# Kernel tuning notes

Hardware: AMD Instinct MI355X
Metric: run time of the kernel (lower is better)

## Reference

```python
import jax, jax.numpy as jnp
import numpy as np

B, LI, LC, H = 16, 2048, 2048, 1024


def setup_inputs() -> dict:
    key = jax.random.key(0)
    k1, k2, k3, k4 = jax.random.split(key, 4)
    inp = jax.random.normal(k1, (B, LI, H), dtype=jnp.float32)
    ctx = jax.random.normal(k2, (B, LC, H), dtype=jnp.float32)
    # mask out the last quarter of context positions (True = masked), never a full row
    context_mask = jnp.broadcast_to(jnp.arange(LC) >= (3 * LC) // 4, (B, LC))
    W = jax.random.normal(k3, (H, H), dtype=jnp.float32) * (1.0 / np.sqrt(H))
    b = jax.random.normal(k4, (H,), dtype=jnp.float32) * 0.01
    return {"input": inp, "context": ctx, "context_mask": context_mask, "W": W, "b": b}


def reference(input, context, context_mask, W, b):
    # shared relu-projected linear for query and key/value sides
    q = jax.nn.relu(jnp.einsum('bih,oh->bio', input, W) + b)    # [B, Li, H]
    k = jax.nn.relu(jnp.einsum('bjh,oh->bjo', context, W) + b)  # [B, Lc, H]
    scores = jnp.einsum('bid,bjd->bij', q, k)                    # [B, Li, Lc], no scaling
    scores = jnp.where(context_mask[:, None, :], -jnp.inf, scores)
    probs = jax.nn.softmax(scores, axis=2)
    return jnp.einsum('bij,bjd->bid', probs, k)                  # weighted sum of context hiddens
```

## Files before the change

kernel.cpp:

```cpp
#include <hip/hip_runtime.h>

typedef _Float16 half8 __attribute__((ext_vector_type(8)));
typedef _Float16 half4 __attribute__((ext_vector_type(4)));
typedef float floatx4 __attribute__((ext_vector_type(4)));

#define OFF_X    0L
#define OFF_S    0L
#define OFF_P    67108864L
#define OFF_W    134217728L
#define OFF_QK   136314880L
#define OFF_KT   270532608L
#define OFF_MASK 337641472L
#define WS_NEED  337674240L

__device__ __forceinline__ void glds16(const void* g, void* l) {
  __builtin_amdgcn_global_load_lds(
      (__attribute__((address_space(1))) void*)(void*)(g),
      (__attribute__((address_space(3))) void*)(l), 16, 0, 0);
}

__global__ void mask_canon(const unsigned* __restrict__ raw,
                           unsigned char* __restrict__ outm) {
  __shared__ int flag;
  int t = threadIdx.x;
  if (t == 0) flag = 0;
  __syncthreads();
  int loc = 0;
  for (int i = t; i < 8192; i += 256)
    if (raw[i] > 1u) loc = 1;
  if (loc) flag = 1;
  __syncthreads();
  if (flag) {
    const unsigned char* b8 = (const unsigned char*)raw;
    for (int j = t; j < 32768; j += 256) outm[j] = (b8[j] != 0);
  } else {
    const int* r32 = (const int*)raw;
    for (int j = t; j < 32768; j += 256) outm[j] = (r32[j] != 0);
  }
}

__global__ __launch_bounds__(256) void cvt_f32_f16(const float* __restrict__ x,
                                                   _Float16* __restrict__ y, long n) {
  long i = ((long)blockIdx.x * 256 + threadIdx.x) * 4;
  if (i + 3 < n) {
    float4 v = *(const float4*)(x + i);
    half4 h;
    h[0] = (_Float16)v.x; h[1] = (_Float16)v.y;
    h[2] = (_Float16)v.z; h[3] = (_Float16)v.w;
    *(half4*)(y + i) = h;
  }
}

template <bool EPI>
__global__ __launch_bounds__(256, 3)
void gemm_nt(const _Float16* __restrict__ A, long sAz,
             const _Float16* __restrict__ B, long sBz,
             void* __restrict__ Cv, long sCz,
             const float* __restrict__ bias, int K, int ldc) {
  __shared__ _Float16 As[128 * 64];
  __shared__ _Float16 Bs[128 * 64];
  const int t = threadIdx.x;
  const int l = t & 63;
  const int w = t >> 6;
  A += (long)blockIdx.z * sAz + (long)blockIdx.y * 128 * K;
  B += (long)blockIdx.z * sBz + (long)blockIdx.x * 128 * K;
  const int waveM = (w >> 1) * 64, waveN = (w & 1) * 64;
  const int l15 = l & 15, quad = l >> 4;
  const int srow = l >> 3;
  const int gchunk = (l & 7) ^ (srow & 7);

  floatx4 acc[4][4] = {};

  for (int kt = 0; kt < K; kt += 64) {
    __syncthreads();
#pragma unroll
    for (int c = 0; c < 4; c++) {
      const int r = w * 32 + c * 8;
      glds16(A + (long)(r + srow) * K + kt + gchunk * 8, As + r * 64);
      glds16(B + (long)(r + srow) * K + kt + gchunk * 8, Bs + r * 64);
    }
    __syncthreads();
#pragma unroll
    for (int k32 = 0; k32 < 2; k32++) {
      half8 af[4], bfr[4];
#pragma unroll
      for (int mi = 0; mi < 4; mi++) {
        const int r = waveM + mi * 16 + l15;
        const int cc = (k32 * 4 + quad) ^ (r & 7);
        af[mi] = *(const half8*)(As + r * 64 + cc * 8);
      }
#pragma unroll
      for (int ni = 0; ni < 4; ni++) {
        const int r = waveN + ni * 16 + l15;
        const int cc = (k32 * 4 + quad) ^ (r & 7);
        bfr[ni] = *(const half8*)(Bs + r * 64 + cc * 8);
      }
#pragma unroll
      for (int mi = 0; mi < 4; mi++)
#pragma unroll
        for (int ni = 0; ni < 4; ni++)
          acc[mi][ni] = __builtin_amdgcn_mfma_f32_16x16x32_f16(af[mi], bfr[ni],
                                                               acc[mi][ni], 0, 0, 0);
    }
  }

  const int rowb = quad * 4;
  if constexpr (EPI) {
    _Float16* Cp = (_Float16*)Cv + (long)blockIdx.z * sCz +
                   (long)blockIdx.y * 128 * ldc + blockIdx.x * 128;
#pragma unroll
    for (int mi = 0; mi < 4; mi++)
#pragma unroll
      for (int ni = 0; ni < 4; ni++) {
        const int col = waveN + ni * 16 + l15;
        const float bv = bias[blockIdx.x * 128 + col];
#pragma unroll
        for (int p = 0; p < 4; p++) {
          const int row = waveM + mi * 16 + rowb + p;
          Cp[(long)row * ldc + col] = (_Float16)fmaxf(acc[mi][ni][p] + bv, 0.f);
        }
      }
  } else {
    float* Cp = (float*)Cv + (long)blockIdx.z * sCz +
                (long)blockIdx.y * 128 * ldc + blockIdx.x * 128;
#pragma unroll
    for (int mi = 0; mi < 4; mi++)
#pragma unroll
      for (int ni = 0; ni < 4; ni++) {
        const int col = waveN + ni * 16 + l15;
#pragma unroll
        for (int p = 0; p < 4; p++) {
          const int row = waveM + mi * 16 + rowb + p;
          Cp[(long)row * ldc + col] = acc[mi][ni][p];
        }
      }
  }
}

__global__ __launch_bounds__(256) void transpose_k(const _Float16* __restrict__ Km,
                                                   _Float16* __restrict__ KT) {
  __shared__ _Float16 tile[64 * 72];
  const int t = threadIdx.x;
  const long b = blockIdx.z;
  const _Float16* src = Km + (b * 2048 + blockIdx.x * 64) * 1024 + blockIdx.y * 64;
  {
    const int jl = t >> 2, hc = (t & 3) * 16;
    half8 v0 = *(const half8*)(src + (long)jl * 1024 + hc);
    half8 v1 = *(const half8*)(src + (long)jl * 1024 + hc + 8);
    *(half8*)&tile[jl * 72 + hc] = v0;
    *(half8*)&tile[jl * 72 + hc + 8] = v1;
  }
  __syncthreads();
  {
    const int hl = t >> 2, jc = (t & 3) * 16;
    half8 o0, o1;
#pragma unroll
    for (int jj = 0; jj < 8; jj++) o0[jj] = tile[(jc + jj) * 72 + hl];
#pragma unroll
    for (int jj = 0; jj < 8; jj++) o1[jj] = tile[(jc + 8 + jj) * 72 + hl];
    long off = (b * 1024 + blockIdx.y * 64 + hl) * 2048 + blockIdx.x * 64 + jc;
    *(half8*)(KT + off) = o0;
    *(half8*)(KT + off + 8) = o1;
  }
}

__global__ __launch_bounds__(256) void softmax_k(const float* __restrict__ S,
                                                 _Float16* __restrict__ P,
                                                 const unsigned char* __restrict__ mask,
                                                 int b0) {
  const int i = blockIdx.x, z = blockIdx.y, t = threadIdx.x;
  const float* s = S + ((long)z * 2048 + i) * 2048;
  const unsigned char* mrow = mask + (long)(b0 + z) * 2048;
  const int base0 = t * 4, base1 = 1024 + t * 4;
  float4 a0 = *(const float4*)(s + base0);
  float4 a1 = *(const float4*)(s + base1);
  float v[8] = {a0.x, a0.y, a0.z, a0.w, a1.x, a1.y, a1.z, a1.w};
  const float NINF = -__builtin_inff();
#pragma unroll
  for (int k = 0; k < 4; k++) {
    if (mrow[base0 + k]) v[k] = NINF;
    if (mrow[base1 + k]) v[4 + k] = NINF;
  }
  float mx = v[0];
#pragma unroll
  for (int k = 1; k < 8; k++) mx = fmaxf(mx, v[k]);
#pragma unroll
  for (int o = 32; o >= 1; o >>= 1) mx = fmaxf(mx, __shfl_xor(mx, o, 64));
  __shared__ float redm[4], reds[4];
  if ((t & 63) == 0) redm[t >> 6] = mx;
  __syncthreads();
  mx = fmaxf(fmaxf(redm[0], redm[1]), fmaxf(redm[2], redm[3]));
  float e[8], sm = 0.f;
#pragma unroll
  for (int k = 0; k < 8; k++) { e[k] = __expf(v[k] - mx); sm += e[k]; }
#pragma unroll
  for (int o = 32; o >= 1; o >>= 1) sm += __shfl_xor(sm, o, 64);
  if ((t & 63) == 0) reds[t >> 6] = sm;
  __syncthreads();
  sm = reds[0] + reds[1] + reds[2] + reds[3];
  const float inv = 1.0f / sm;
  _Float16* p = P + ((long)z * 2048 + i) * 2048;
  half4 h0, h1;
#pragma unroll
  for (int k = 0; k < 4; k++) { h0[k] = (_Float16)(e[k] * inv); h1[k] = (_Float16)(e[4 + k] * inv); }
  *(half4*)(p + base0) = h0;
  *(half4*)(p + base1) = h1;
}

extern "C" void kernel_launch(void* const* d_in, const int* in_sizes, int n_in,
                              void* d_out, int out_size, void* d_ws, size_t ws_size,
                              hipStream_t stream) {
  (void)in_sizes; (void)n_in; (void)out_size;
  if ((long)ws_size < WS_NEED) return;

  const float* inp  = (const float*)d_in[0];
  const float* ctx  = (const float*)d_in[1];
  const unsigned* msk = (const unsigned*)d_in[2];
  const float* W    = (const float*)d_in[3];
  const float* bias = (const float*)d_in[4];
  float* out = (float*)d_out;
  char* ws = (char*)d_ws;

  _Float16* Xf   = (_Float16*)(ws + OFF_X);
  float*    Sb   = (float*)(ws + OFF_S);
  _Float16* Pb   = (_Float16*)(ws + OFF_P);
  _Float16* Wf   = (_Float16*)(ws + OFF_W);
  _Float16* QK   = (_Float16*)(ws + OFF_QK);
  _Float16* KT   = (_Float16*)(ws + OFF_KT);
  unsigned char* Mc = (unsigned char*)(ws + OFF_MASK);

  mask_canon<<<1, 256, 0, stream>>>(msk, Mc);
  cvt_f32_f16<<<32768, 256, 0, stream>>>(inp, Xf, 33554432L);
  cvt_f32_f16<<<32768, 256, 0, stream>>>(ctx, Xf + 33554432L, 33554432L);
  cvt_f32_f16<<<1024, 256, 0, stream>>>(W, Wf, 1048576L);
  gemm_nt<true><<<dim3(8, 512, 1), 256, 0, stream>>>(Xf, 0L, Wf, 0L, (void*)QK, 0L,
                                                     bias, 1024, 1024);
  transpose_k<<<dim3(32, 16, 16), 256, 0, stream>>>(QK + 32768L * 1024, KT);
  for (int bp = 0; bp < 4; bp++) {
    const _Float16* Aq = QK + (long)bp * 4 * 2048 * 1024;
    const _Float16* Bk = QK + (32768L + (long)bp * 4 * 2048) * 1024;
    gemm_nt<false><<<dim3(16, 16, 4), 256, 0, stream>>>(Aq, 2048L * 1024, Bk, 2048L * 1024,
                                                        (void*)Sb, 2048L * 2048, nullptr,
                                                        1024, 2048);
    softmax_k<<<dim3(2048, 4), 256, 0, stream>>>(Sb, Pb, Mc, bp * 4);
    gemm_nt<false><<<dim3(8, 16, 4), 256, 0, stream>>>(Pb, 2048L * 2048,
                                                       KT + (long)bp * 4 * 1024 * 2048,
                                                       1024L * 2048,
                                                       (void*)(out + (long)bp * 4 * 2048 * 1024),
                                                       2048L * 1024, nullptr, 2048, 1024);
  }
}
```

Baseline: 1.012 ms.

## Use 256x256 double-buffered 8-wave GEMM with phased prefetch and batched PV

Replaces the 128x128 single-buffered GEMM with a 512-thread, 256x256-tile kernel. A and B tiles are double-buffered in LDS, and global-to-LDS prefetches are interleaved with four MFMA phases using s_setprio and explicit waitcnt/barriers. The aim is to raise arithmetic intensity and hide load latency. The attention loop now runs two QK/softmax passes into a larger probability buffer before one PV GEMM over 8 batches, which gives more blocks per launch. The cost is 128KB of LDS per block, so only one block fits per CU, plus tighter synchronisation logic.

```diff
diff --git a/kernel.cpp b/kernel.cpp
--- a/kernel.cpp
+++ b/kernel.cpp
@@ -52,85 +52,133 @@
 }
 
 template <bool EPI>
-__global__ __launch_bounds__(256, 3)
-void gemm_nt(const _Float16* __restrict__ A, long sAz,
-             const _Float16* __restrict__ B, long sBz,
-             void* __restrict__ Cv, long sCz,
-             const float* __restrict__ bias, int K, int ldc) {
-  __shared__ _Float16 As[128 * 64];
-  __shared__ _Float16 Bs[128 * 64];
+__global__ __launch_bounds__(512, 2)
+void gemm_nt8(const _Float16* __restrict__ A, long sAz,
+              const _Float16* __restrict__ B, long sBz,
+              void* __restrict__ Cv, long sCz,
+              const float* __restrict__ bias, int K, int ldc) {
+  __shared__ _Float16 As[2][256 * 64];
+  __shared__ _Float16 Bs[2][256 * 64];
   const int t = threadIdx.x;
   const int l = t & 63;
   const int w = t >> 6;
-  A += (long)blockIdx.z * sAz + (long)blockIdx.y * 128 * K;
-  B += (long)blockIdx.z * sBz + (long)blockIdx.x * 128 * K;
-  const int waveM = (w >> 1) * 64, waveN = (w & 1) * 64;
+  const int wr = w >> 2, wc = w & 3;
+  A += (long)blockIdx.z * sAz + (long)blockIdx.y * 256 * (long)K;
+  B += (long)blockIdx.z * sBz + (long)blockIdx.x * 256 * (long)K;
   const int l15 = l & 15, quad = l >> 4;
   const int srow = l >> 3;
   const int gchunk = (l & 7) ^ (srow & 7);
-
-  floatx4 acc[4][4] = {};
-
-  for (int kt = 0; kt < K; kt += 64) {
-    __syncthreads();
-#pragma unroll
-    for (int c = 0; c < 4; c++) {
-      const int r = w * 32 + c * 8;
-      glds16(A + (long)(r + srow) * K + kt + gchunk * 8, As + r * 64);
-      glds16(B + (long)(r + srow) * K + kt + gchunk * 8, Bs + r * 64);
+  const int sbase = w * 8;
+  const int cc0 = quad ^ (l15 & 7);
+  const int aoff0 = (wr * 128 + l15) * 64 + cc0 * 8;
+  const int aoff1 = (wr * 128 + l15) * 64 + (cc0 ^ 4) * 8;
+  const int boff0 = (wc * 64 + l15) * 64 + cc0 * 8;
+  const int boff1 = (wc * 64 + l15) * 64 + (cc0 ^ 4) * 8;
+
+  floatx4 acc[8][4] = {};
+  const int NT = K >> 6;
+
+#define STG(src, dst, rnd, kt)                                                   \
+  glds16((src) + (long)((rnd) * 64 + sbase + srow) * K + (kt) + gchunk * 8,      \
+         (dst) + ((rnd) * 64 + sbase) * 64)
+
+  STG(A, As[0], 0, 0); STG(A, As[0], 1, 0); STG(A, As[0], 2, 0); STG(A, As[0], 3, 0);
+  STG(B, Bs[0], 0, 0); STG(B, Bs[0], 1, 0); STG(B, Bs[0], 2, 0); STG(B, Bs[0], 3, 0);
+  {
+    const int k1 = (NT > 1) ? 64 : 0;
+    STG(B, Bs[1], 0, k1); STG(B, Bs[1], 1, k1); STG(B, Bs[1], 2, k1); STG(B, Bs[1], 3, k1);
+  }
+
+#define READ_A(afv, m0)                                           \
+  afv[0][0] = *(const half8*)(Ap + aoff0 + (m0) * 1024);          \
+  afv[0][1] = *(const half8*)(Ap + aoff1 + (m0) * 1024);          \
+  afv[1][0] = *(const half8*)(Ap + aoff0 + ((m0) + 1) * 1024);    \
+  afv[1][1] = *(const half8*)(Ap + aoff1 + ((m0) + 1) * 1024);
+
+#define PHASE_TAIL(m0, afv)                                                                                \
+  __builtin_amdgcn_s_barrier();                                                                            \
+  asm volatile("s_waitcnt lgkmcnt(0)" ::: "memory");                                                       \
+  __builtin_amdgcn_s_setprio(1);                                                                           \
+  _Pragma("unroll")                                                                                        \
+  for (int ni = 0; ni < 4; ++ni) {                                                                         \
+    acc[m0][ni] = __builtin_amdgcn_mfma_f32_16x16x32_f16(afv[0][0], bf[ni][0], acc[m0][ni], 0, 0, 0);      \
+    acc[m0][ni] = __builtin_amdgcn_mfma_f32_16x16x32_f16(afv[0][1], bf[ni][1], acc[m0][ni], 0, 0, 0);      \
+    acc[(m0) + 1][ni] =                                                                                    \
+        __builtin_amdgcn_mfma_f32_16x16x32_f16(afv[1][0], bf[ni][0], acc[(m0) + 1][ni], 0, 0, 0);          \
+    acc[(m0) + 1][ni] =                                                                                    \
+        __builtin_amdgcn_mfma_f32_16x16x32_f16(afv[1][1], bf[ni][1], acc[(m0) + 1][ni], 0, 0, 0);          \
+  }                                                                                                        \
+  __builtin_amdgcn_s_setprio(0);                                                                           \
+  __builtin_amdgcn_s_barrier();
+
+  for (int tt = 0; tt < NT; ++tt) {
+    const _Float16* Ap = As[tt & 1];
+    const _Float16* Bp = Bs[tt & 1];
+    _Float16* Anx = As[(tt + 1) & 1];
+    _Float16* Bnx = Bs[tt & 1];
+    const int kt1 = ((tt + 1 < NT) ? tt + 1 : NT - 1) * 64;
+    const int kt2 = ((tt + 2 < NT) ? tt + 2 : NT - 1) * 64;
+
+    asm volatile("s_waitcnt vmcnt(4)" ::: "memory");
+    __builtin_amdgcn_s_barrier();
+    asm volatile("" ::: "memory");
+
+    half8 bf[4][2], af0[2][2], af1[2][2];
+#pragma unroll
+    for (int ni = 0; ni < 4; ++ni) {
+      bf[ni][0] = *(const half8*)(Bp + boff0 + ni * 1024);
+      bf[ni][1] = *(const half8*)(Bp + boff1 + ni * 1024);
     }
-    __syncthreads();
-#pragma unroll
-    for (int k32 = 0; k32 < 2; k32++) {
-      half8 af[4], bfr[4];
-#pragma unroll
-      for (int mi = 0; mi < 4; mi++) {
-        const int r = waveM + mi * 16 + l15;
-        const int cc = (k32 * 4 + quad) ^ (r & 7);
-        af[mi] = *(const half8*)(As + r * 64 + cc * 8);
-      }
-#pragma unroll
-      for (int ni = 0; ni < 4; ni++) {
-        const int r = waveN + ni * 16 + l15;
-        const int cc = (k32 * 4 + quad) ^ (r & 7);
-        bfr[ni] = *(const half8*)(Bs + r * 64 + cc * 8);
-      }
-#pragma unroll
-      for (int mi = 0; mi < 4; mi++)
-#pragma unroll
-        for (int ni = 0; ni < 4; ni++)
-          acc[mi][ni] = __builtin_amdgcn_mfma_f32_16x16x32_f16(af[mi], bfr[ni],
-                                                               acc[mi][ni], 0, 0, 0);
-    }
-  }
+    READ_A(af0, 0)
+    STG(A, Anx, 0, kt1);
+    STG(A, Anx, 1, kt1);
+    PHASE_TAIL(0, af0)
+    READ_A(af1, 2)
+    STG(A, Anx, 2, kt1);
+    STG(A, Anx, 3, kt1);
+    PHASE_TAIL(2, af1)
+    READ_A(af0, 4)
+    STG(B, Bnx, 0, kt2);
+    STG(B, Bnx, 1, kt2);
+    PHASE_TAIL(4, af0)
+    READ_A(af1, 6)
+    STG(B, Bnx, 2, kt2);
+    STG(B, Bnx, 3, kt2);
+    PHASE_TAIL(6, af1)
+  }
+  asm volatile("s_waitcnt vmcnt(0)" ::: "memory");
+#undef STG
+#undef READ_A
+#undef PHASE_TAIL
 
   const int rowb = quad * 4;
+  const long cbase = (long)blockIdx.z * sCz + (long)blockIdx.y * 256 * (long)ldc + blockIdx.x * 256;
   if constexpr (EPI) {
-    _Float16* Cp = (_Float16*)Cv + (long)blockIdx.z * sCz +
-                   (long)blockIdx.y * 128 * ldc + blockIdx.x * 128;
-#pragma unroll
-    for (int mi = 0; mi < 4; mi++)
-#pragma unroll
-      for (int ni = 0; ni < 4; ni++) {
-        const int col = waveN + ni * 16 + l15;
-        const float bv = bias[blockIdx.x * 128 + col];
-#pragma unroll
-        for (int p = 0; p < 4; p++) {
-          const int row = waveM + mi * 16 + rowb + p;
-          Cp[(long)row * ldc + col] = (_Float16)fmaxf(acc[mi][ni][p] + bv, 0.f);
+    _Float16* Cp = (_Float16*)Cv + cbase;
+    float bv[4];
+#pragma unroll
+    for (int ni = 0; ni < 4; ++ni) bv[ni] = bias[blockIdx.x * 256 + wc * 64 + ni * 16 + l15];
+#pragma unroll
+    for (int mi = 0; mi < 8; ++mi)
+#pragma unroll
+      for (int ni = 0; ni < 4; ++ni) {
+        const int col = wc * 64 + ni * 16 + l15;
+#pragma unroll
+        for (int p = 0; p < 4; ++p) {
+          const int row = wr * 128 + mi * 16 + rowb + p;
+          Cp[(long)row * ldc + col] = (_Float16)fmaxf(acc[mi][ni][p] + bv[ni], 0.f);
         }
       }
   } else {
-    float* Cp = (float*)Cv + (long)blockIdx.z * sCz +
-                (long)blockIdx.y * 128 * ldc + blockIdx.x * 128;
-#pragma unroll
-    for (int mi = 0; mi < 4; mi++)
-#pragma unroll
-      for (int ni = 0; ni < 4; ni++) {
-        const int col = waveN + ni * 16 + l15;
-#pragma unroll
-        for (int p = 0; p < 4; p++) {
-          const int row = waveM + mi * 16 + rowb + p;
+    float* Cp = (float*)Cv + cbase;
+#pragma unroll
+    for (int mi = 0; mi < 8; ++mi)
+#pragma unroll
+      for (int ni = 0; ni < 4; ++ni) {
+        const int col = wc * 64 + ni * 16 + l15;
+#pragma unroll
+        for (int p = 0; p < 4; ++p) {
+          const int row = wr * 128 + mi * 16 + rowb + p;
           Cp[(long)row * ldc + col] = acc[mi][ni][p];
         }
       }
@@ -233,20 +281,23 @@
   cvt_f32_f16<<<32768, 256, 0, stream>>>(inp, Xf, 33554432L);
   cvt_f32_f16<<<32768, 256, 0, stream>>>(ctx, Xf + 33554432L, 33554432L);
   cvt_f32_f16<<<1024, 256, 0, stream>>>(W, Wf, 1048576L);
-  gemm_nt<true><<<dim3(8, 512, 1), 256, 0, stream>>>(Xf, 0L, Wf, 0L, (void*)QK, 0L,
-                                                     bias, 1024, 1024);
+  gemm_nt8<true><<<dim3(4, 256, 1), 512, 0, stream>>>(Xf, 0L, Wf, 0L, (void*)QK, 0L,
+                                                      bias, 1024, 1024);
   transpose_k<<<dim3(32, 16, 16), 256, 0, stream>>>(QK + 32768L * 1024, KT);
-  for (int bp = 0; bp < 4; bp++) {
-    const _Float16* Aq = QK + (long)bp * 4 * 2048 * 1024;
-    const _Float16* Bk = QK + (32768L + (long)bp * 4 * 2048) * 1024;
-    gemm_nt<false><<<dim3(16, 16, 4), 256, 0, stream>>>(Aq, 2048L * 1024, Bk, 2048L * 1024,
-                                                        (void*)Sb, 2048L * 2048, nullptr,
-                                                        1024, 2048);
-    softmax_k<<<dim3(2048, 4), 256, 0, stream>>>(Sb, Pb, Mc, bp * 4);
-    gemm_nt<false><<<dim3(8, 16, 4), 256, 0, stream>>>(Pb, 2048L * 2048,
-                                                       KT + (long)bp * 4 * 1024 * 2048,
+  for (int g = 0; g < 2; g++) {
+    for (int q = 0; q < 2; q++) {
+      const int bp = g * 2 + q;
+      const _Float16* Aq = QK + (long)bp * 4 * 2048 * 1024;
+      const _Float16* Bk = QK + (32768L + (long)bp * 4 * 2048) * 1024;
+      gemm_nt8<false><<<dim3(8, 8, 4), 512, 0, stream>>>(Aq, 2048L * 1024, Bk, 2048L * 1024,
+                                                         (void*)Sb, 2048L * 2048, nullptr,
+                                                         1024, 2048);
+      softmax_k<<<dim3(2048, 4), 256, 0, stream>>>(Sb, Pb + (long)q * 4 * 2048 * 2048, Mc, bp * 4);
+    }
+    gemm_nt8<false><<<dim3(4, 8, 8), 512, 0, stream>>>(Pb, 2048L * 2048,
+                                                       KT + (long)g * 8 * 1024 * 2048,
                                                        1024L * 2048,
-                                                       (void*)(out + (long)bp * 4 * 2048 * 1024),
+                                                       (void*)(out + (long)g * 8 * 2048 * 1024),
                                                        2048L * 1024, nullptr, 2048, 1024);
   }
 }
```

Result: faster. 984.2 us (-2.8%).
